# Kernel optimization log

Measured on AMD Instinct MI355X. Metric: run time of the kernel, lower is better.

The kernel has to match this reference:

```python
import jax, jax.numpy as jnp
import numpy as np

EPS = 1e-7  # keras backend.epsilon()
NUM_ROUTING = 3


def squash(v, axis=-1):
    s2 = jnp.sum(jnp.square(v), axis=axis, keepdims=True)
    scale = s2 / (1.0 + s2) / jnp.sqrt(s2 + EPS)
    return scale * v


def setup_inputs() -> dict:
    key = jax.random.key(0)
    k1, k2 = jax.random.split(key)
    B, J, I, P, Q = 64, 32, 2048, 32, 16
    inputs = jax.random.normal(k1, (B, I, Q), dtype=jnp.float32)
    # glorot_uniform for W [J, I, P, Q]
    fan_in, fan_out = Q, P
    limit = np.sqrt(6.0 / (fan_in + fan_out))
    W = jax.random.uniform(k2, (J, I, P, Q), dtype=jnp.float32, minval=-limit, maxval=limit)
    return {"inputs": inputs, "W": W}


def reference(inputs, W):
    # prediction vectors: u_hat[b,j,i,p] = sum_q inputs[b,i,q] * W[j,i,p,q]
    inputs_hat = jnp.einsum('biq,jipq->bjip', inputs, W)  # [B,J,I,P]
    inputs_hat_stop = jax.lax.stop_gradient(inputs_hat)
    B, J, I, _ = inputs_hat.shape
    b = jnp.zeros((B, J, I), dtype=inputs_hat.dtype)
    for _ in range(NUM_ROUTING - 1):
        c = jax.nn.softmax(b, axis=1)  # softmax over output capsules j
        v = squash(jnp.einsum('bji,bjip->bjp', c, inputs_hat_stop))
        b = b + jnp.einsum('bjp,bjip->bji', v, inputs_hat_stop)
    c = jax.nn.softmax(b, axis=1)
    return squash(jnp.einsum('bji,bjip->bjp', c, inputs_hat))  # [B,J,P]
```

## Files before the change

kernel.cpp:

```cpp
#include <hip/hip_runtime.h>


namespace {

using bfrag = __attribute__((ext_vector_type(8))) short;
using ffrag = __attribute__((ext_vector_type(4))) float;

constexpr int I_DIM = 2048;
constexpr int B_DIM = 64;
constexpr int N_DIM = 1024;
constexpr int TI    = 16;

__device__ __forceinline__ unsigned short f2bf(float f) {
    unsigned int u = __float_as_uint(f);
    unsigned int r = (u + 0x7fffu + ((u >> 16) & 1u)) >> 16;
    return (unsigned short)r;
}

template<int CTRL>
__device__ __forceinline__ float dppf(float x) {
    return __int_as_float(
        __builtin_amdgcn_update_dpp(0, __float_as_int(x), CTRL, 0xF, 0xF, true));
}
__device__ __forceinline__ float sum16(float x) {
    x += dppf<0x121>(x);
    x += dppf<0x122>(x);
    x += dppf<0x124>(x);
    x += dppf<0x128>(x);
    return x;
}
__device__ __forceinline__ float max16(float x) {
    x = fmaxf(x, dppf<0x121>(x));
    x = fmaxf(x, dppf<0x122>(x));
    x = fmaxf(x, dppf<0x124>(x));
    x = fmaxf(x, dppf<0x128>(x));
    return x;
}


__global__ __launch_bounds__(256)
void conv_w(const float* __restrict__ W, unsigned short* __restrict__ Wt) {
    const int t = blockIdx.x * 256 + threadIdx.x;
    const int i = t >> 10, n = t & 1023;
    const float* src = W + ((((n >> 5) * I_DIM + i) * 32 + (n & 31)) << 4);
    unsigned int o[8];
    #pragma unroll
    for (int k = 0; k < 8; ++k)
        o[k] = (unsigned int)f2bf(src[2 * k]) | ((unsigned int)f2bf(src[2 * k + 1]) << 16);
    uint4* dst = reinterpret_cast<uint4*>(Wt + (size_t)t * 16);
    dst[0] = make_uint4(o[0], o[1], o[2], o[3]);
    dst[1] = make_uint4(o[4], o[5], o[6], o[7]);
}

__global__ __launch_bounds__(256)
void conv_x(const float* __restrict__ x, unsigned short* __restrict__ xT2) {
    const int t = blockIdx.x * 256 + threadIdx.x;
    const int i = t >> 6, b = t & 63;
    const float* src = x + (((size_t)b * I_DIM + i) << 4);
    unsigned int o[16];
    #pragma unroll
    for (int k = 0; k < 8; ++k) {
        const float f0 = src[2 * k], f1 = src[2 * k + 1];
        const unsigned short h0 = f2bf(f0), h1 = f2bf(f1);
        const float l0 = f0 - __uint_as_float(((unsigned int)h0) << 16);
        const float l1 = f1 - __uint_as_float(((unsigned int)h1) << 16);
        o[k]     = (unsigned int)h0       | ((unsigned int)h1 << 16);
        o[8 + k] = (unsigned int)f2bf(l0) | ((unsigned int)f2bf(l1) << 16);
    }
    uint4* dst = reinterpret_cast<uint4*>(xT2 + (size_t)t * 32);
    #pragma unroll
    for (int k = 0; k < 4; ++k)
        dst[k] = make_uint4(o[4 * k], o[4 * k + 1], o[4 * k + 2], o[4 * k + 3]);
}

#define LOAD_FRAGS(iv)                                                          \
    do {                                                                        \
        const int i_ = (iv);                                                    \
        af = *reinterpret_cast<const bfrag*>(                                   \
            xT2 + (((size_t)i_ << 6) + b0 + li) * 32 + g8);                     \
        _Pragma("unroll")                                                       \
        for (int t = 0; t < 4; ++t)                                             \
            bfr[t] = *reinterpret_cast<const bfrag*>(                           \
                Wt + (((size_t)i_ << 10) + ((j0 + (t >> 1)) << 5)               \
                      + ((t & 1) << 4) + li) * 16 + qb);                        \
    } while (0)

template<bool ROUTED>
__global__ __launch_bounds__(1024, 4)
void caps_pass(const unsigned short* __restrict__ Wt,
               const unsigned short* __restrict__ xT2,
               const float* __restrict__ v_in,
               float* __restrict__ s_out)
{
    __shared__ float d_buf[16 * 33];
    __shared__ float c_buf[16 * 33];

    const int tid = threadIdx.x;
    const int w   = tid >> 6;
    const int l   = tid & 63;
    const int g   = l >> 4;
    const int li  = l & 15;
    const int j0  = w << 1;
    const int qb  = (g & 1) << 3;
    const int g8  = g << 3;

    const int bid = (int)blockIdx.x;
    const int V   = (bid & 7) * 64 + (bid >> 3);
    const int it  = V >> 2;
    const int b0  = (V & 3) << 4;

    float vr[4][4];
    if (ROUTED) {
        #pragma unroll
        for (int r = 0; r < 4; ++r)
            #pragma unroll
            for (int t = 0; t < 4; ++t)
                vr[r][t] = v_in[((b0 + (g << 2) + r) * 32 + j0 + (t >> 1)) * 32
                                + ((t & 1) << 4) + li];
    }

    bfrag af;
    bfrag bfr[4];
    LOAD_FRAGS(it * TI);

    ffrag s[4];
    #pragma unroll
    for (int t = 0; t < 4; ++t) s[t] = ffrag{0.f, 0.f, 0.f, 0.f};

    for (int ii = 0; ii < TI; ++ii) {
        ffrag u[4];
        #pragma unroll
        for (int t = 0; t < 4; ++t) {
            ffrag z{0.f, 0.f, 0.f, 0.f};
            u[t] = __builtin_amdgcn_mfma_f32_16x16x32_bf16(af, bfr[t], z, 0, 0, 0);
        }

        LOAD_FRAGS(it * TI + ((ii + 1 < TI) ? (ii + 1) : ii));
        asm volatile("" ::: "memory");

        if (ROUTED) {
            float dsel[4];
            #pragma unroll
            for (int r = 0; r < 4; ++r) {
                float d0 = u[0][r] * vr[r][0] + u[1][r] * vr[r][1];
                float d1 = u[2][r] * vr[r][2] + u[3][r] * vr[r][3];
                d0 = sum16(d0);
                d1 = sum16(d1);
                dsel[r] = (li & 1) ? d1 : d0;
            }
            #pragma unroll
            for (int r = 0; r < 4; ++r)
                if (li < 2) d_buf[((g << 2) + r) * 33 + j0 + li] = dsel[r];

            asm volatile("s_waitcnt lgkmcnt(0)\n\ts_barrier" ::: "memory");

            if (tid < 512) {
                const int bl = tid >> 5, jx = tid & 31;
                const float bn = d_buf[bl * 33 + jx];
                float m = max16(bn);
                m = fmaxf(m, __shfl_xor(m, 16));
                const float e = __expf(bn - m);
                float ssum = sum16(e);
                ssum += __shfl_xor(ssum, 16);
                c_buf[bl * 33 + jx] = e / ssum;
            }

            asm volatile("s_waitcnt lgkmcnt(0)\n\ts_barrier" ::: "memory");

            #pragma unroll
            for (int r = 0; r < 4; ++r) {
                const float c0 = c_buf[((g << 2) + r) * 33 + j0];
                const float c1 = c_buf[((g << 2) + r) * 33 + j0 + 1];
                s[0][r] += c0 * u[0][r];
                s[1][r] += c0 * u[1][r];
                s[2][r] += c1 * u[2][r];
                s[3][r] += c1 * u[3][r];
            }
        } else {
            #pragma unroll
            for (int t = 0; t < 4; ++t) s[t] += u[t];
        }
    }

    const float sc = ROUTED ? 1.f : (1.f / 32.f);
    #pragma unroll
    for (int t = 0; t < 4; ++t)
        #pragma unroll
        for (int r = 0; r < 4; ++r)
            atomicAdd(&s_out[(b0 + (g << 2) + r) * N_DIM
                             + ((j0 + (t >> 1)) << 5) + ((t & 1) << 4) + li],
                      s[t][r] * sc);
}

__global__ __launch_bounds__(256)
void squash_add(const float* __restrict__ s, const float* __restrict__ base,
                float* __restrict__ dst) {
    const int t = blockIdx.x * 256 + threadIdx.x;
    if (t >= B_DIM * 32) return;
    const float* sp = s + t * 32;
    float n2 = 0.f;
    #pragma unroll
    for (int p = 0; p < 32; ++p) { const float xv = sp[p]; n2 += xv * xv; }
    const float scl = n2 / ((1.f + n2) * sqrtf(n2 + 1e-7f));
    float* op = dst + t * 32;
    #pragma unroll
    for (int p = 0; p < 32; ++p)
        op[p] = (base ? base[t * 32 + p] : 0.f) + scl * sp[p];
}

}

extern "C" void kernel_launch(void* const* d_in, const int* in_sizes, int n_in,
                              void* d_out, int out_size, void* d_ws, size_t ws_size,
                              hipStream_t stream) {
    const float* x = (const float*)d_in[0];
    const float* W = (const float*)d_in[1];
    float* out = (float*)d_out;

    const size_t needW = (size_t)I_DIM * N_DIM * 16 * 2;
    const size_t needX = (size_t)I_DIM * B_DIM * 32 * 2;
    const size_t needS = (size_t)B_DIM * N_DIM * 4;

    char* p = (char*)d_ws;
    unsigned short* Wt  = (unsigned short*)p; p += needW;
    unsigned short* xT2 = (unsigned short*)p; p += needX;
    float* s  = (float*)p; p += needS;
    float* v1 = (float*)p; p += needS;
    float* vs = (float*)p;

    conv_x<<<(I_DIM * B_DIM) / 256, 256, 0, stream>>>(x, xT2);
    conv_w<<<(I_DIM * N_DIM) / 256, 256, 0, stream>>>(W, Wt);

    const dim3 rg(512), rb(1024);

    hipMemsetAsync(s, 0, needS, stream);
    caps_pass<false><<<rg, rb, 0, stream>>>(Wt, xT2, nullptr, s);
    squash_add<<<8, 256, 0, stream>>>(s, nullptr, v1);

    hipMemsetAsync(s, 0, needS, stream);
    caps_pass<true><<<rg, rb, 0, stream>>>(Wt, xT2, v1, s);
    squash_add<<<8, 256, 0, stream>>>(s, v1, vs);

    hipMemsetAsync(s, 0, needS, stream);
    caps_pass<true><<<rg, rb, 0, stream>>>(Wt, xT2, vs, s);
    squash_add<<<8, 256, 0, stream>>>(s, nullptr, out);
}
```

Before: 255.5 us.

## Fuse W bf16 conversion into first pass, batch routing by two i, drop atomics

The separate conv_w kernel is removed. The first (unrouted) capsule pass now reads fp32 W directly, converts it to bf16 in registers, and writes the converted tiles for later passes. Routed passes process two i-rows per barrier pair to halve synchronisation, and a 1024-thread softmax covers 32 rows. Atomic accumulation and the memsets are replaced by per-tile partial sums that a new squash_reduce kernel sums, at the cost of a 32MB partial buffer written and read each pass.

```diff
diff --git a/kernel.cpp b/kernel.cpp
--- a/kernel.cpp
+++ b/kernel.cpp
@@ -10,11 +10,11 @@
 constexpr int B_DIM = 64;
 constexpr int N_DIM = 1024;
 constexpr int TI    = 16;
+constexpr int NIT   = I_DIM / TI;
 
 __device__ __forceinline__ unsigned short f2bf(float f) {
     unsigned int u = __float_as_uint(f);
-    unsigned int r = (u + 0x7fffu + ((u >> 16) & 1u)) >> 16;
-    return (unsigned short)r;
+    return (unsigned short)((u + 0x7fffu + ((u >> 16) & 1u)) >> 16);
 }
 
 template<int CTRL>
@@ -23,33 +23,14 @@
         __builtin_amdgcn_update_dpp(0, __float_as_int(x), CTRL, 0xF, 0xF, true));
 }
 __device__ __forceinline__ float sum16(float x) {
-    x += dppf<0x121>(x);
-    x += dppf<0x122>(x);
-    x += dppf<0x124>(x);
-    x += dppf<0x128>(x);
+    x += dppf<0x121>(x); x += dppf<0x122>(x);
+    x += dppf<0x124>(x); x += dppf<0x128>(x);
     return x;
 }
 __device__ __forceinline__ float max16(float x) {
-    x = fmaxf(x, dppf<0x121>(x));
-    x = fmaxf(x, dppf<0x122>(x));
-    x = fmaxf(x, dppf<0x124>(x));
-    x = fmaxf(x, dppf<0x128>(x));
+    x = fmaxf(x, dppf<0x121>(x)); x = fmaxf(x, dppf<0x122>(x));
+    x = fmaxf(x, dppf<0x124>(x)); x = fmaxf(x, dppf<0x128>(x));
     return x;
-}
-
-
-__global__ __launch_bounds__(256)
-void conv_w(const float* __restrict__ W, unsigned short* __restrict__ Wt) {
-    const int t = blockIdx.x * 256 + threadIdx.x;
-    const int i = t >> 10, n = t & 1023;
-    const float* src = W + ((((n >> 5) * I_DIM + i) * 32 + (n & 31)) << 4);
-    unsigned int o[8];
-    #pragma unroll
-    for (int k = 0; k < 8; ++k)
-        o[k] = (unsigned int)f2bf(src[2 * k]) | ((unsigned int)f2bf(src[2 * k + 1]) << 16);
-    uint4* dst = reinterpret_cast<uint4*>(Wt + (size_t)t * 16);
-    dst[0] = make_uint4(o[0], o[1], o[2], o[3]);
-    dst[1] = make_uint4(o[4], o[5], o[6], o[7]);
 }
 
 __global__ __launch_bounds__(256)
@@ -73,27 +54,16 @@
         dst[k] = make_uint4(o[4 * k], o[4 * k + 1], o[4 * k + 2], o[4 * k + 3]);
 }
 
-#define LOAD_FRAGS(iv)                                                          \
-    do {                                                                        \
-        const int i_ = (iv);                                                    \
-        af = *reinterpret_cast<const bfrag*>(                                   \
-            xT2 + (((size_t)i_ << 6) + b0 + li) * 32 + g8);                     \
-        _Pragma("unroll")                                                       \
-        for (int t = 0; t < 4; ++t)                                             \
-            bfr[t] = *reinterpret_cast<const bfrag*>(                           \
-                Wt + (((size_t)i_ << 10) + ((j0 + (t >> 1)) << 5)               \
-                      + ((t & 1) << 4) + li) * 16 + qb);                        \
-    } while (0)
-
 template<bool ROUTED>
-__global__ __launch_bounds__(1024, 4)
-void caps_pass(const unsigned short* __restrict__ Wt,
+__global__ __launch_bounds__(1024)
+void caps_pass(const float* __restrict__ Wf,
+               unsigned short* __restrict__ Wt,
                const unsigned short* __restrict__ xT2,
                const float* __restrict__ v_in,
-               float* __restrict__ s_out)
+               float* __restrict__ s_part)
 {
-    __shared__ float d_buf[16 * 33];
-    __shared__ float c_buf[16 * 33];
+    __shared__ float d_buf[32 * 33];
+    __shared__ float c_buf[32 * 33];
 
     const int tid = threadIdx.x;
     const int w   = tid >> 6;
@@ -109,76 +79,120 @@
     const int it  = V >> 2;
     const int b0  = (V & 3) << 4;
 
-    float vr[4][4];
-    if (ROUTED) {
+    const unsigned short* pa = xT2 + (b0 + li) * 32 + g8;
+
+    ffrag s[4];
+    #pragma unroll
+    for (int t = 0; t < 4; ++t) s[t] = ffrag{0.f, 0.f, 0.f, 0.f};
+
+    if constexpr (ROUTED) {
+        float vr[4][4];
         #pragma unroll
         for (int r = 0; r < 4; ++r)
             #pragma unroll
             for (int t = 0; t < 4; ++t)
                 vr[r][t] = v_in[((b0 + (g << 2) + r) * 32 + j0 + (t >> 1)) * 32
                                 + ((t & 1) << 4) + li];
-    }
-
-    bfrag af;
-    bfrag bfr[4];
-    LOAD_FRAGS(it * TI);
-
-    ffrag s[4];
-    #pragma unroll
-    for (int t = 0; t < 4; ++t) s[t] = ffrag{0.f, 0.f, 0.f, 0.f};
-
-    for (int ii = 0; ii < TI; ++ii) {
-        ffrag u[4];
-        #pragma unroll
-        for (int t = 0; t < 4; ++t) {
-            ffrag z{0.f, 0.f, 0.f, 0.f};
-            u[t] = __builtin_amdgcn_mfma_f32_16x16x32_bf16(af, bfr[t], z, 0, 0, 0);
+
+        const unsigned short* pb[4];
+        #pragma unroll
+        for (int t = 0; t < 4; ++t)
+            pb[t] = Wt + (size_t)((((j0 + (t >> 1)) << 5) + ((t & 1) << 4) + li) * 16 + qb);
+
+        bfrag afn[2], bfn[2][4];
+        #pragma unroll
+        for (int ic = 0; ic < 2; ++ic) {
+            const size_t i0 = (size_t)(it * TI + ic);
+            afn[ic] = *reinterpret_cast<const bfrag*>(pa + (i0 << 11));
+            #pragma unroll
+            for (int t = 0; t < 4; ++t)
+                bfn[ic][t] = *reinterpret_cast<const bfrag*>(pb[t] + (i0 << 14));
         }
 
-        LOAD_FRAGS(it * TI + ((ii + 1 < TI) ? (ii + 1) : ii));
-        asm volatile("" ::: "memory");
-
-        if (ROUTED) {
-            float dsel[4];
-            #pragma unroll
-            for (int r = 0; r < 4; ++r) {
-                float d0 = u[0][r] * vr[r][0] + u[1][r] * vr[r][1];
-                float d1 = u[2][r] * vr[r][2] + u[3][r] * vr[r][3];
-                d0 = sum16(d0);
-                d1 = sum16(d1);
-                dsel[r] = (li & 1) ? d1 : d0;
+        for (int cc = 0; cc < TI / 2; ++cc) {
+            ffrag u[2][4];
+            #pragma unroll
+            for (int ic = 0; ic < 2; ++ic)
+                #pragma unroll
+                for (int t = 0; t < 4; ++t) {
+                    ffrag z{0.f, 0.f, 0.f, 0.f};
+                    u[ic][t] = __builtin_amdgcn_mfma_f32_16x16x32_bf16(
+                        afn[ic], bfn[ic][t], z, 0, 0, 0);
+                }
+
+            const int inext = it * TI + ((cc < TI / 2 - 1) ? 2 * cc + 2 : 2 * cc);
+            #pragma unroll
+            for (int ic = 0; ic < 2; ++ic) {
+                const size_t i0 = (size_t)(inext + ic);
+                afn[ic] = *reinterpret_cast<const bfrag*>(pa + (i0 << 11));
+                #pragma unroll
+                for (int t = 0; t < 4; ++t)
+                    bfn[ic][t] = *reinterpret_cast<const bfrag*>(pb[t] + (i0 << 14));
             }
-            #pragma unroll
-            for (int r = 0; r < 4; ++r)
-                if (li < 2) d_buf[((g << 2) + r) * 33 + j0 + li] = dsel[r];
+            asm volatile("" ::: "memory");
+
+            #pragma unroll
+            for (int ic = 0; ic < 2; ++ic)
+                #pragma unroll
+                for (int r = 0; r < 4; ++r) {
+                    float d0 = u[ic][0][r] * vr[r][0] + u[ic][1][r] * vr[r][1];
+                    float d1 = u[ic][2][r] * vr[r][2] + u[ic][3][r] * vr[r][3];
+                    d0 = sum16(d0);
+                    d1 = sum16(d1);
+                    const float dsel = (li & 1) ? d1 : d0;
+                    if (li < 2)
+                        d_buf[((ic << 4) + (g << 2) + r) * 33 + j0 + li] = dsel;
+                }
 
             asm volatile("s_waitcnt lgkmcnt(0)\n\ts_barrier" ::: "memory");
 
-            if (tid < 512) {
-                const int bl = tid >> 5, jx = tid & 31;
-                const float bn = d_buf[bl * 33 + jx];
+            {
+                const int row = tid >> 5, jx = tid & 31;
+                const float bn = d_buf[row * 33 + jx];
                 float m = max16(bn);
                 m = fmaxf(m, __shfl_xor(m, 16));
                 const float e = __expf(bn - m);
                 float ssum = sum16(e);
                 ssum += __shfl_xor(ssum, 16);
-                c_buf[bl * 33 + jx] = e / ssum;
+                c_buf[row * 33 + jx] = e / ssum;
             }
 
             asm volatile("s_waitcnt lgkmcnt(0)\n\ts_barrier" ::: "memory");
 
             #pragma unroll
-            for (int r = 0; r < 4; ++r) {
-                const float c0 = c_buf[((g << 2) + r) * 33 + j0];
-                const float c1 = c_buf[((g << 2) + r) * 33 + j0 + 1];
-                s[0][r] += c0 * u[0][r];
-                s[1][r] += c0 * u[1][r];
-                s[2][r] += c1 * u[2][r];
-                s[3][r] += c1 * u[3][r];
+            for (int ic = 0; ic < 2; ++ic)
+                #pragma unroll
+                for (int r = 0; r < 4; ++r) {
+                    const float c0 = c_buf[((ic << 4) + (g << 2) + r) * 33 + j0];
+                    const float c1 = c_buf[((ic << 4) + (g << 2) + r) * 33 + j0 + 1];
+                    s[0][r] += c0 * u[ic][0][r];
+                    s[1][r] += c0 * u[ic][1][r];
+                    s[2][r] += c1 * u[ic][2][r];
+                    s[3][r] += c1 * u[ic][3][r];
+                }
+        }
+    } else {
+        for (int ii = 0; ii < TI; ++ii) {
+            const int i = it * TI + ii;
+            const bfrag a = *reinterpret_cast<const bfrag*>(pa + ((size_t)i << 11));
+            #pragma unroll
+            for (int t = 0; t < 4; ++t) {
+                const int jj = j0 + (t >> 1);
+                const int nl = ((t & 1) << 4) + li;
+                const float* wp = Wf + (((size_t)jj * I_DIM + i) << 9) + nl * 16 + qb;
+                const float4 wa = reinterpret_cast<const float4*>(wp)[0];
+                const float4 wb = reinterpret_cast<const float4*>(wp)[1];
+                bfrag bf;
+                bf[0] = (short)f2bf(wa.x); bf[1] = (short)f2bf(wa.y);
+                bf[2] = (short)f2bf(wa.z); bf[3] = (short)f2bf(wa.w);
+                bf[4] = (short)f2bf(wb.x); bf[5] = (short)f2bf(wb.y);
+                bf[6] = (short)f2bf(wb.z); bf[7] = (short)f2bf(wb.w);
+                if (b0 == 0 && g < 2) {
+                    *reinterpret_cast<bfrag*>(
+                        Wt + ((((size_t)i << 10) + (jj << 5) + nl) << 4) + qb) = bf;
+                }
+                s[t] = __builtin_amdgcn_mfma_f32_16x16x32_bf16(a, bf, s[t], 0, 0, 0);
             }
-        } else {
-            #pragma unroll
-            for (int t = 0; t < 4; ++t) s[t] += u[t];
         }
     }
 
@@ -187,25 +201,32 @@
     for (int t = 0; t < 4; ++t)
         #pragma unroll
         for (int r = 0; r < 4; ++r)
-            atomicAdd(&s_out[(b0 + (g << 2) + r) * N_DIM
-                             + ((j0 + (t >> 1)) << 5) + ((t & 1) << 4) + li],
-                      s[t][r] * sc);
+            s_part[((size_t)it * B_DIM + b0 + (g << 2) + r) * N_DIM
+                   + ((j0 + (t >> 1)) << 5) + ((t & 1) << 4) + li] = s[t][r] * sc;
 }
 
 __global__ __launch_bounds__(256)
-void squash_add(const float* __restrict__ s, const float* __restrict__ base,
-                float* __restrict__ dst) {
-    const int t = blockIdx.x * 256 + threadIdx.x;
-    if (t >= B_DIM * 32) return;
-    const float* sp = s + t * 32;
-    float n2 = 0.f;
-    #pragma unroll
-    for (int p = 0; p < 32; ++p) { const float xv = sp[p]; n2 += xv * xv; }
+void squash_reduce(const float* __restrict__ s_part,
+                   const float* __restrict__ base,
+                   float* __restrict__ dst) {
+    const int tid = threadIdx.x;
+    const int rr  = blockIdx.x * 8 + (tid >> 5);
+    const int p   = tid & 31;
+    const int b   = rr >> 5, j = rr & 31;
+    const float* sp = s_part + (size_t)b * N_DIM + (j << 5) + p;
+    float a0 = 0.f, a1 = 0.f, a2 = 0.f, a3 = 0.f;
+    for (int it2 = 0; it2 < NIT; it2 += 4) {
+        a0 += sp[(size_t)(it2 + 0) << 16];
+        a1 += sp[(size_t)(it2 + 1) << 16];
+        a2 += sp[(size_t)(it2 + 2) << 16];
+        a3 += sp[(size_t)(it2 + 3) << 16];
+    }
+    const float sv = (a0 + a1) + (a2 + a3);
+    float n2 = sv * sv;
+    n2 = sum16(n2);
+    n2 += __shfl_xor(n2, 16);
     const float scl = n2 / ((1.f + n2) * sqrtf(n2 + 1e-7f));
-    float* op = dst + t * 32;
-    #pragma unroll
-    for (int p = 0; p < 32; ++p)
-        op[p] = (base ? base[t * 32 + p] : 0.f) + scl * sp[p];
+    dst[rr * 32 + p] = (base ? base[rr * 32 + p] : 0.f) + scl * sv;
 }
 
 }
@@ -219,29 +240,28 @@
 
     const size_t needW = (size_t)I_DIM * N_DIM * 16 * 2;
     const size_t needX = (size_t)I_DIM * B_DIM * 32 * 2;
-    const size_t needS = (size_t)B_DIM * N_DIM * 4;
-
-    char* p = (char*)d_ws;
-    unsigned short* Wt  = (unsigned short*)p; p += needW;
-    unsigned short* xT2 = (unsigned short*)p; p += needX;
-    float* s  = (float*)p; p += needS;
-    float* v1 = (float*)p; p += needS;
-    float* vs = (float*)p;
+    const size_t needP = (size_t)NIT * B_DIM * N_DIM * 4;
+    const size_t needV = (size_t)B_DIM * N_DIM * 4;
+
+    char* pp = (char*)d_ws;
+    unsigned short* Wt  = (unsigned short*)pp; pp += needW;
+    unsigned short* xT2 = (unsigned short*)pp; pp += needX;
+    float* s_part = (float*)pp; pp += needP;
+    float* v1     = (float*)pp; pp += needV;
+    float* vs     = (float*)pp;
+    (void)needX; (void)ws_size;
 
     conv_x<<<(I_DIM * B_DIM) / 256, 256, 0, stream>>>(x, xT2);
-    conv_w<<<(I_DIM * N_DIM) / 256, 256, 0, stream>>>(W, Wt);
 
     const dim3 rg(512), rb(1024);
-
-    hipMemsetAsync(s, 0, needS, stream);
-    caps_pass<false><<<rg, rb, 0, stream>>>(Wt, xT2, nullptr, s);
-    squash_add<<<8, 256, 0, stream>>>(s, nullptr, v1);
-
-    hipMemsetAsync(s, 0, needS, stream);
-    caps_pass<true><<<rg, rb, 0, stream>>>(Wt, xT2, v1, s);
-    squash_add<<<8, 256, 0, stream>>>(s, v1, vs);
-
-    hipMemsetAsync(s, 0, needS, stream);
-    caps_pass<true><<<rg, rb, 0, stream>>>(Wt, xT2, vs, s);
-    squash_add<<<8, 256, 0, stream>>>(s, nullptr, out);
-}
+    const dim3 qg(256), qb(256);
+
+    caps_pass<false><<<rg, rb, 0, stream>>>(W, Wt, xT2, nullptr, s_part);
+    squash_reduce<<<qg, qb, 0, stream>>>(s_part, nullptr, v1);
+
+    caps_pass<true><<<rg, rb, 0, stream>>>(W, Wt, xT2, v1, s_part);
+    squash_reduce<<<qg, qb, 0, stream>>>(s_part, v1, vs);
+
+    caps_pass<true><<<rg, rb, 0, stream>>>(W, Wt, xT2, vs, s_part);
+    squash_reduce<<<qg, qb, 0, stream>>>(s_part, nullptr, out);
+}
```

Result: slower. 335.0 us (+31.1%).

## Split routed pass into agreement, softmax, and weighted-sum sweeps without block barriers

Applied to the files above, without the earlier changes.

The routed pass used to compute agreement, softmax over output capsules, and the weighted sum inside one kernel, with two block barriers per input-capsule step. It is now split into three kernels. The first computes agreement logits and writes them to a global buffer, a separate kernel applies the softmax, and the second sweep recomputes the prediction vectors and accumulates them with the precomputed coefficients. This removes the per-step barriers and shared-memory traffic. In exchange it makes one extra full MFMA sweep over W per routing iteration and adds round trips through several MB of global memory. The unrouted pass also now accumulates directly in the MFMA accumulator, and addressing uses precomputed base pointers.

```diff
diff --git a/kernel.cpp b/kernel.cpp
--- a/kernel.cpp
+++ b/kernel.cpp
@@ -13,8 +13,7 @@
 
 __device__ __forceinline__ unsigned short f2bf(float f) {
     unsigned int u = __float_as_uint(f);
-    unsigned int r = (u + 0x7fffu + ((u >> 16) & 1u)) >> 16;
-    return (unsigned short)r;
+    return (unsigned short)((u + 0x7fffu + ((u >> 16) & 1u)) >> 16);
 }
 
 template<int CTRL>
@@ -23,17 +22,13 @@
         __builtin_amdgcn_update_dpp(0, __float_as_int(x), CTRL, 0xF, 0xF, true));
 }
 __device__ __forceinline__ float sum16(float x) {
-    x += dppf<0x121>(x);
-    x += dppf<0x122>(x);
-    x += dppf<0x124>(x);
-    x += dppf<0x128>(x);
+    x += dppf<0x121>(x); x += dppf<0x122>(x);
+    x += dppf<0x124>(x); x += dppf<0x128>(x);
     return x;
 }
 __device__ __forceinline__ float max16(float x) {
-    x = fmaxf(x, dppf<0x121>(x));
-    x = fmaxf(x, dppf<0x122>(x));
-    x = fmaxf(x, dppf<0x124>(x));
-    x = fmaxf(x, dppf<0x128>(x));
+    x = fmaxf(x, dppf<0x121>(x)); x = fmaxf(x, dppf<0x122>(x));
+    x = fmaxf(x, dppf<0x124>(x)); x = fmaxf(x, dppf<0x128>(x));
     return x;
 }
 
@@ -75,26 +70,22 @@
 
 #define LOAD_FRAGS(iv)                                                          \
     do {                                                                        \
-        const int i_ = (iv);                                                    \
-        af = *reinterpret_cast<const bfrag*>(                                   \
-            xT2 + (((size_t)i_ << 6) + b0 + li) * 32 + g8);                     \
+        const size_t i_ = (size_t)(iv);                                         \
+        af = *reinterpret_cast<const bfrag*>(pa + (i_ << 11));                  \
         _Pragma("unroll")                                                       \
         for (int t = 0; t < 4; ++t)                                             \
-            bfr[t] = *reinterpret_cast<const bfrag*>(                           \
-                Wt + (((size_t)i_ << 10) + ((j0 + (t >> 1)) << 5)               \
-                      + ((t & 1) << 4) + li) * 16 + qb);                        \
+            bfr[t] = *reinterpret_cast<const bfrag*>(pb[t] + (i_ << 14));       \
     } while (0)
 
-template<bool ROUTED>
-__global__ __launch_bounds__(1024, 4)
-void caps_pass(const unsigned short* __restrict__ Wt,
-               const unsigned short* __restrict__ xT2,
-               const float* __restrict__ v_in,
-               float* __restrict__ s_out)
+template<int MODE>
+__global__ __launch_bounds__(1024)
+void caps_sweep(const unsigned short* __restrict__ Wt,
+                const unsigned short* __restrict__ xT2,
+                const float* __restrict__ v_in,
+                const float* __restrict__ c_in,
+                float* __restrict__ d_out,
+                float* __restrict__ s_out)
 {
-    __shared__ float d_buf[16 * 33];
-    __shared__ float c_buf[16 * 33];
-
     const int tid = threadIdx.x;
     const int w   = tid >> 6;
     const int l   = tid & 63;
@@ -109,8 +100,14 @@
     const int it  = V >> 2;
     const int b0  = (V & 3) << 4;
 
+    const unsigned short* pa = xT2 + (b0 + li) * 32 + g8;
+    const unsigned short* pb[4];
+    #pragma unroll
+    for (int t = 0; t < 4; ++t)
+        pb[t] = Wt + (size_t)((((j0 + (t >> 1)) << 5) + ((t & 1) << 4) + li) * 16 + qb);
+
     float vr[4][4];
-    if (ROUTED) {
+    if (MODE == 1) {
         #pragma unroll
         for (int r = 0; r < 4; ++r)
             #pragma unroll
@@ -128,68 +125,79 @@
     for (int t = 0; t < 4; ++t) s[t] = ffrag{0.f, 0.f, 0.f, 0.f};
 
     for (int ii = 0; ii < TI; ++ii) {
-        ffrag u[4];
+        const int i = it * TI + ii;
+
+        float2 cw[4];
+        if (MODE == 2) {
+            #pragma unroll
+            for (int r = 0; r < 4; ++r)
+                cw[r] = *reinterpret_cast<const float2*>(
+                    c_in + ((size_t)i * B_DIM + b0 + (g << 2) + r) * 32 + j0);
+        }
+
+        if (MODE == 0) {
+            #pragma unroll
+            for (int t = 0; t < 4; ++t)
+                s[t] = __builtin_amdgcn_mfma_f32_16x16x32_bf16(af, bfr[t], s[t], 0, 0, 0);
+            LOAD_FRAGS(it * TI + ((ii + 1 < TI) ? ii + 1 : ii));
+            asm volatile("" ::: "memory");
+        } else {
+            ffrag u[4];
+            #pragma unroll
+            for (int t = 0; t < 4; ++t) {
+                ffrag z{0.f, 0.f, 0.f, 0.f};
+                u[t] = __builtin_amdgcn_mfma_f32_16x16x32_bf16(af, bfr[t], z, 0, 0, 0);
+            }
+            LOAD_FRAGS(it * TI + ((ii + 1 < TI) ? ii + 1 : ii));
+            asm volatile("" ::: "memory");
+
+            if (MODE == 1) {
+                #pragma unroll
+                for (int r = 0; r < 4; ++r) {
+                    float d0 = u[0][r] * vr[r][0] + u[1][r] * vr[r][1];
+                    float d1 = u[2][r] * vr[r][2] + u[3][r] * vr[r][3];
+                    d0 = sum16(d0);
+                    d1 = sum16(d1);
+                    const float dsel = (li & 1) ? d1 : d0;
+                    if (li < 2)
+                        d_out[((size_t)i * B_DIM + b0 + (g << 2) + r) * 32 + j0 + li] = dsel;
+                }
+            } else {
+                #pragma unroll
+                for (int r = 0; r < 4; ++r) {
+                    s[0][r] += cw[r].x * u[0][r];
+                    s[1][r] += cw[r].x * u[1][r];
+                    s[2][r] += cw[r].y * u[2][r];
+                    s[3][r] += cw[r].y * u[3][r];
+                }
+            }
+        }
+    }
+
+    if (MODE != 1) {
+        const float sc = (MODE == 0) ? (1.f / 32.f) : 1.f;
         #pragma unroll
-        for (int t = 0; t < 4; ++t) {
-            ffrag z{0.f, 0.f, 0.f, 0.f};
-            u[t] = __builtin_amdgcn_mfma_f32_16x16x32_bf16(af, bfr[t], z, 0, 0, 0);
-        }
-
-        LOAD_FRAGS(it * TI + ((ii + 1 < TI) ? (ii + 1) : ii));
-        asm volatile("" ::: "memory");
-
-        if (ROUTED) {
-            float dsel[4];
-            #pragma unroll
-            for (int r = 0; r < 4; ++r) {
-                float d0 = u[0][r] * vr[r][0] + u[1][r] * vr[r][1];
-                float d1 = u[2][r] * vr[r][2] + u[3][r] * vr[r][3];
-                d0 = sum16(d0);
-                d1 = sum16(d1);
-                dsel[r] = (li & 1) ? d1 : d0;
-            }
+        for (int t = 0; t < 4; ++t)
             #pragma unroll
             for (int r = 0; r < 4; ++r)
-                if (li < 2) d_buf[((g << 2) + r) * 33 + j0 + li] = dsel[r];
-
-            asm volatile("s_waitcnt lgkmcnt(0)\n\ts_barrier" ::: "memory");
-
-            if (tid < 512) {
-                const int bl = tid >> 5, jx = tid & 31;
-                const float bn = d_buf[bl * 33 + jx];
-                float m = max16(bn);
-                m = fmaxf(m, __shfl_xor(m, 16));
-                const float e = __expf(bn - m);
-                float ssum = sum16(e);
-                ssum += __shfl_xor(ssum, 16);
-                c_buf[bl * 33 + jx] = e / ssum;
-            }
-
-            asm volatile("s_waitcnt lgkmcnt(0)\n\ts_barrier" ::: "memory");
-
-            #pragma unroll
-            for (int r = 0; r < 4; ++r) {
-                const float c0 = c_buf[((g << 2) + r) * 33 + j0];
-                const float c1 = c_buf[((g << 2) + r) * 33 + j0 + 1];
-                s[0][r] += c0 * u[0][r];
-                s[1][r] += c0 * u[1][r];
-                s[2][r] += c1 * u[2][r];
-                s[3][r] += c1 * u[3][r];
-            }
-        } else {
-            #pragma unroll
-            for (int t = 0; t < 4; ++t) s[t] += u[t];
-        }
-    }
-
-    const float sc = ROUTED ? 1.f : (1.f / 32.f);
-    #pragma unroll
-    for (int t = 0; t < 4; ++t)
-        #pragma unroll
-        for (int r = 0; r < 4; ++r)
-            atomicAdd(&s_out[(b0 + (g << 2) + r) * N_DIM
-                             + ((j0 + (t >> 1)) << 5) + ((t & 1) << 4) + li],
-                      s[t][r] * sc);
+                atomicAdd(&s_out[(b0 + (g << 2) + r) * N_DIM
+                                 + ((j0 + (t >> 1)) << 5) + ((t & 1) << 4) + li],
+                          s[t][r] * sc);
+    }
+}
+
+__global__ __launch_bounds__(1024)
+void softmax_c(const float* __restrict__ d, float* __restrict__ c) {
+    const int tid = threadIdx.x;
+    const size_t row = (size_t)blockIdx.x * 32 + (tid >> 5);
+    const int jx = tid & 31;
+    const float bn = d[row * 32 + jx];
+    float m = max16(bn);
+    m = fmaxf(m, __shfl_xor(m, 16));
+    const float e = __expf(bn - m);
+    float ssum = sum16(e);
+    ssum += __shfl_xor(ssum, 16);
+    c[row * 32 + jx] = e / ssum;
 }
 
 __global__ __launch_bounds__(256)
@@ -219,29 +227,38 @@
 
     const size_t needW = (size_t)I_DIM * N_DIM * 16 * 2;
     const size_t needX = (size_t)I_DIM * B_DIM * 32 * 2;
+    const size_t needD = (size_t)I_DIM * B_DIM * 32 * 4;
     const size_t needS = (size_t)B_DIM * N_DIM * 4;
 
-    char* p = (char*)d_ws;
-    unsigned short* Wt  = (unsigned short*)p; p += needW;
-    unsigned short* xT2 = (unsigned short*)p; p += needX;
-    float* s  = (float*)p; p += needS;
-    float* v1 = (float*)p; p += needS;
-    float* vs = (float*)p;
+    char* pp = (char*)d_ws;
+    unsigned short* Wt  = (unsigned short*)pp; pp += needW;
+    unsigned short* xT2 = (unsigned short*)pp; pp += needX;
+    float* dbuf = (float*)pp; pp += needD;
+    float* cbuf = (float*)pp; pp += needD;
+    float* s    = (float*)pp; pp += needS;
+    float* v1   = (float*)pp; pp += needS;
+    float* vs   = (float*)pp;
+    (void)ws_size;
 
     conv_x<<<(I_DIM * B_DIM) / 256, 256, 0, stream>>>(x, xT2);
     conv_w<<<(I_DIM * N_DIM) / 256, 256, 0, stream>>>(W, Wt);
 
     const dim3 rg(512), rb(1024);
+    const dim3 sg(I_DIM * B_DIM / 32), sb(1024);
 
     hipMemsetAsync(s, 0, needS, stream);
-    caps_pass<false><<<rg, rb, 0, stream>>>(Wt, xT2, nullptr, s);
+    caps_sweep<0><<<rg, rb, 0, stream>>>(Wt, xT2, nullptr, nullptr, nullptr, s);
     squash_add<<<8, 256, 0, stream>>>(s, nullptr, v1);
 
+    caps_sweep<1><<<rg, rb, 0, stream>>>(Wt, xT2, v1, nullptr, dbuf, nullptr);
+    softmax_c<<<sg, sb, 0, stream>>>(dbuf, cbuf);
     hipMemsetAsync(s, 0, needS, stream);
-    caps_pass<true><<<rg, rb, 0, stream>>>(Wt, xT2, v1, s);
+    caps_sweep<2><<<rg, rb, 0, stream>>>(Wt, xT2, nullptr, cbuf, nullptr, s);
     squash_add<<<8, 256, 0, stream>>>(s, v1, vs);
 
+    caps_sweep<1><<<rg, rb, 0, stream>>>(Wt, xT2, vs, nullptr, dbuf, nullptr);
+    softmax_c<<<sg, sb, 0, stream>>>(dbuf, cbuf);
     hipMemsetAsync(s, 0, needS, stream);
-    caps_pass<true><<<rg, rb, 0, stream>>>(Wt, xT2, vs, s);
+    caps_sweep<2><<<rg, rb, 0, stream>>>(Wt, xT2, nullptr, cbuf, nullptr, s);
     squash_add<<<8, 256, 0, stream>>>(s, nullptr, out);
 }
```

New measurement: 354.2 us. +38.6%, slower.

## Stage W and x tiles into LDS with async double-buffered global_load_lds

Applied to the files above, without the earlier changes.

Replaces per-wave direct global fragment loads with a double-buffered LDS staging pipeline that uses global_load_lds, and repacks W and x in the conversion kernels so each stage is a contiguous copy. Blocks shrink to 512 threads, with each wave handling 4 output capsules (8 MFMA tiles). The unrouted pass now accumulates directly through the MFMA accumulator, and the softmax is spread across all waves. The aim is to hide global memory latency and reduce redundant fragment loads, at the cost of more LDS, more registers and manual vmcnt bookkeeping.

```diff
diff --git a/kernel.cpp b/kernel.cpp
--- a/kernel.cpp
+++ b/kernel.cpp
@@ -13,8 +13,7 @@
 
 __device__ __forceinline__ unsigned short f2bf(float f) {
     unsigned int u = __float_as_uint(f);
-    unsigned int r = (u + 0x7fffu + ((u >> 16) & 1u)) >> 16;
-    return (unsigned short)r;
+    return (unsigned short)((u + 0x7fffu + ((u >> 16) & 1u)) >> 16);
 }
 
 template<int CTRL>
@@ -23,18 +22,26 @@
         __builtin_amdgcn_update_dpp(0, __float_as_int(x), CTRL, 0xF, 0xF, true));
 }
 __device__ __forceinline__ float sum16(float x) {
-    x += dppf<0x121>(x);
-    x += dppf<0x122>(x);
-    x += dppf<0x124>(x);
-    x += dppf<0x128>(x);
+    x += dppf<0x121>(x); x += dppf<0x122>(x);
+    x += dppf<0x124>(x); x += dppf<0x128>(x);
     return x;
 }
 __device__ __forceinline__ float max16(float x) {
-    x = fmaxf(x, dppf<0x121>(x));
-    x = fmaxf(x, dppf<0x122>(x));
-    x = fmaxf(x, dppf<0x124>(x));
-    x = fmaxf(x, dppf<0x128>(x));
+    x = fmaxf(x, dppf<0x121>(x)); x = fmaxf(x, dppf<0x122>(x));
+    x = fmaxf(x, dppf<0x124>(x)); x = fmaxf(x, dppf<0x128>(x));
     return x;
+}
+
+__device__ __forceinline__ void gl2lds16(const void* gsrc, void* ldst) {
+    __builtin_amdgcn_global_load_lds(
+        (const __attribute__((address_space(1))) void*)gsrc,
+        (__attribute__((address_space(3))) void*)ldst, 16, 0, 0);
+}
+
+__device__ __forceinline__ void barrier_lgkm() {
+    asm volatile("s_waitcnt lgkmcnt(0)" ::: "memory");
+    __builtin_amdgcn_s_barrier();
+    __builtin_amdgcn_sched_barrier(0);
 }
 
 
@@ -47,9 +54,10 @@
     #pragma unroll
     for (int k = 0; k < 8; ++k)
         o[k] = (unsigned int)f2bf(src[2 * k]) | ((unsigned int)f2bf(src[2 * k + 1]) << 16);
-    uint4* dst = reinterpret_cast<uint4*>(Wt + (size_t)t * 16);
-    dst[0] = make_uint4(o[0], o[1], o[2], o[3]);
-    dst[1] = make_uint4(o[4], o[5], o[6], o[7]);
+    uint4* d0 = reinterpret_cast<uint4*>(Wt + (((size_t)i * 2 + 0) * 1024 + n) * 8);
+    uint4* d1 = reinterpret_cast<uint4*>(Wt + (((size_t)i * 2 + 1) * 1024 + n) * 8);
+    *d0 = make_uint4(o[0], o[1], o[2], o[3]);
+    *d1 = make_uint4(o[4], o[5], o[6], o[7]);
 }
 
 __global__ __launch_bounds__(256)
@@ -67,129 +75,147 @@
         o[k]     = (unsigned int)h0       | ((unsigned int)h1 << 16);
         o[8 + k] = (unsigned int)f2bf(l0) | ((unsigned int)f2bf(l1) << 16);
     }
-    uint4* dst = reinterpret_cast<uint4*>(xT2 + (size_t)t * 32);
-    #pragma unroll
-    for (int k = 0; k < 4; ++k)
-        dst[k] = make_uint4(o[4 * k], o[4 * k + 1], o[4 * k + 2], o[4 * k + 3]);
-}
-
-#define LOAD_FRAGS(iv)                                                          \
-    do {                                                                        \
-        const int i_ = (iv);                                                    \
-        af = *reinterpret_cast<const bfrag*>(                                   \
-            xT2 + (((size_t)i_ << 6) + b0 + li) * 32 + g8);                     \
-        _Pragma("unroll")                                                       \
-        for (int t = 0; t < 4; ++t)                                             \
-            bfr[t] = *reinterpret_cast<const bfrag*>(                           \
-                Wt + (((size_t)i_ << 10) + ((j0 + (t >> 1)) << 5)               \
-                      + ((t & 1) << 4) + li) * 16 + qb);                        \
-    } while (0)
-
-template<bool ROUTED>
-__global__ __launch_bounds__(1024, 4)
-void caps_pass(const unsigned short* __restrict__ Wt,
-               const unsigned short* __restrict__ xT2,
-               const float* __restrict__ v_in,
-               float* __restrict__ s_out)
+    #pragma unroll
+    for (int g = 0; g < 4; ++g) {
+        uint4* dst = reinterpret_cast<uint4*>(xT2 + (((size_t)i * 4 + g) * 64 + b) * 8);
+        *dst = make_uint4(o[4 * g], o[4 * g + 1], o[4 * g + 2], o[4 * g + 3]);
+    }
+}
+
+#define WAITC() do { if (w == 7) asm volatile("s_waitcnt vmcnt(5)" ::: "memory"); \
+                     else        asm volatile("s_waitcnt vmcnt(4)" ::: "memory"); } while (0)
+
+template<int ROUTED>
+__global__ __launch_bounds__(512, 2)
+void caps_fused(const unsigned short* __restrict__ Wt,
+                const unsigned short* __restrict__ xT2,
+                const float* __restrict__ v_in,
+                float* __restrict__ s_out)
 {
-    __shared__ float d_buf[16 * 33];
-    __shared__ float c_buf[16 * 33];
+    __shared__ short wbuf[2][16384];
+    __shared__ short xbuf[2][512];
+    __shared__ float d_buf[16 * 36];
+    __shared__ float c_buf[16 * 36];
 
     const int tid = threadIdx.x;
     const int w   = tid >> 6;
     const int l   = tid & 63;
     const int g   = l >> 4;
     const int li  = l & 15;
-    const int j0  = w << 1;
-    const int qb  = (g & 1) << 3;
-    const int g8  = g << 3;
+    const int j0  = w << 2;
 
     const int bid = (int)blockIdx.x;
     const int V   = (bid & 7) * 64 + (bid >> 3);
     const int it  = V >> 2;
     const int b0  = (V & 3) << 4;
-
-    float vr[4][4];
+    const int i0  = it * TI;
+
+    float vr[4][8];
     if (ROUTED) {
         #pragma unroll
         for (int r = 0; r < 4; ++r)
             #pragma unroll
-            for (int t = 0; t < 4; ++t)
+            for (int t = 0; t < 8; ++t)
                 vr[r][t] = v_in[((b0 + (g << 2) + r) * 32 + j0 + (t >> 1)) * 32
                                 + ((t & 1) << 4) + li];
-    }
-
-    bfrag af;
-    bfrag bfr[4];
-    LOAD_FRAGS(it * TI);
-
-    ffrag s[4];
-    #pragma unroll
-    for (int t = 0; t < 4; ++t) s[t] = ffrag{0.f, 0.f, 0.f, 0.f};
+        asm volatile("s_waitcnt vmcnt(0)" ::: "memory");
+    }
+
+    auto stage = [&](int i, int bufn) {
+        const unsigned short* wsrc = Wt + ((size_t)i << 14);
+        #pragma unroll
+        for (int k = 0; k < 4; ++k) {
+            const int c = (w << 2) + k;
+            gl2lds16(wsrc + (c << 9) + (l << 3), &wbuf[bufn][c << 9]);
+        }
+        if (w == 7)
+            gl2lds16(xT2 + (((size_t)i << 2) + (l >> 4)) * 512 + ((b0 + (l & 15)) << 3),
+                     &xbuf[bufn][0]);
+    };
+
+    stage(i0, 0);
+    stage(i0 + 1, 1);
+    WAITC();
+    __builtin_amdgcn_s_barrier();
+    __builtin_amdgcn_sched_barrier(0);
+
+    ffrag s[8];
+    #pragma unroll
+    for (int t = 0; t < 8; ++t) s[t] = ffrag{0.f, 0.f, 0.f, 0.f};
 
     for (int ii = 0; ii < TI; ++ii) {
-        ffrag u[4];
-        #pragma unroll
-        for (int t = 0; t < 4; ++t) {
-            ffrag z{0.f, 0.f, 0.f, 0.f};
-            u[t] = __builtin_amdgcn_mfma_f32_16x16x32_bf16(af, bfr[t], z, 0, 0, 0);
-        }
-
-        LOAD_FRAGS(it * TI + ((ii + 1 < TI) ? (ii + 1) : ii));
-        asm volatile("" ::: "memory");
+        const int cur = ii & 1;
+
+        const bfrag a = *reinterpret_cast<const bfrag*>(&xbuf[cur][((g << 4) + li) << 3]);
+        ffrag u[8];
+        #pragma unroll
+        for (int t = 0; t < 8; ++t) {
+            const int n0 = ((j0 + (t >> 1)) << 5) + ((t & 1) << 4);
+            const bfrag bt = *reinterpret_cast<const bfrag*>(
+                &wbuf[cur][((g & 1) << 13) + ((n0 + li) << 3)]);
+            if (ROUTED) {
+                ffrag z{0.f, 0.f, 0.f, 0.f};
+                u[t] = __builtin_amdgcn_mfma_f32_16x16x32_bf16(a, bt, z, 0, 0, 0);
+            } else {
+                s[t] = __builtin_amdgcn_mfma_f32_16x16x32_bf16(a, bt, s[t], 0, 0, 0);
+            }
+        }
 
         if (ROUTED) {
-            float dsel[4];
             #pragma unroll
             for (int r = 0; r < 4; ++r) {
                 float d0 = u[0][r] * vr[r][0] + u[1][r] * vr[r][1];
                 float d1 = u[2][r] * vr[r][2] + u[3][r] * vr[r][3];
-                d0 = sum16(d0);
-                d1 = sum16(d1);
-                dsel[r] = (li & 1) ? d1 : d0;
+                float d2 = u[4][r] * vr[r][4] + u[5][r] * vr[r][5];
+                float d3 = u[6][r] * vr[r][6] + u[7][r] * vr[r][7];
+                d0 = sum16(d0); d1 = sum16(d1); d2 = sum16(d2); d3 = sum16(d3);
+                float sel = d0;
+                sel = (li == 1) ? d1 : sel;
+                sel = (li == 2) ? d2 : sel;
+                sel = (li == 3) ? d3 : sel;
+                if (li < 4) d_buf[((g << 2) + r) * 36 + j0 + li] = sel;
             }
-            #pragma unroll
-            for (int r = 0; r < 4; ++r)
-                if (li < 2) d_buf[((g << 2) + r) * 33 + j0 + li] = dsel[r];
-
-            asm volatile("s_waitcnt lgkmcnt(0)\n\ts_barrier" ::: "memory");
-
-            if (tid < 512) {
-                const int bl = tid >> 5, jx = tid & 31;
-                const float bn = d_buf[bl * 33 + jx];
-                float m = max16(bn);
-                m = fmaxf(m, __shfl_xor(m, 16));
-                const float e = __expf(bn - m);
-                float ssum = sum16(e);
-                ssum += __shfl_xor(ssum, 16);
-                c_buf[bl * 33 + jx] = e / ssum;
-            }
-
-            asm volatile("s_waitcnt lgkmcnt(0)\n\ts_barrier" ::: "memory");
+        }
+        barrier_lgkm();
+
+        if (ii + 2 < TI) stage(i0 + ii + 2, cur);
+
+        if (ROUTED) {
+            const int row = (w << 1) + (l >> 5), jx = l & 31;
+            const float dv = d_buf[row * 36 + jx];
+            float m = max16(dv);
+            m = fmaxf(m, __shfl_xor(m, 16));
+            const float e = __expf(dv - m);
+            float sm = sum16(e);
+            sm += __shfl_xor(sm, 16);
+            c_buf[row * 36 + jx] = e / sm;
+            barrier_lgkm();
 
             #pragma unroll
             for (int r = 0; r < 4; ++r) {
-                const float c0 = c_buf[((g << 2) + r) * 33 + j0];
-                const float c1 = c_buf[((g << 2) + r) * 33 + j0 + 1];
-                s[0][r] += c0 * u[0][r];
-                s[1][r] += c0 * u[1][r];
-                s[2][r] += c1 * u[2][r];
-                s[3][r] += c1 * u[3][r];
+                const ffrag cr = *reinterpret_cast<const ffrag*>(
+                    &c_buf[((g << 2) + r) * 36 + j0]);
+                #pragma unroll
+                for (int t = 0; t < 8; ++t)
+                    s[t][r] += cr[t >> 1] * u[t][r];
             }
-        } else {
-            #pragma unroll
-            for (int t = 0; t < 4; ++t) s[t] += u[t];
-        }
+        }
+
+        if (ii + 2 < TI) WAITC();
+        else             asm volatile("s_waitcnt vmcnt(0)" ::: "memory");
+        __builtin_amdgcn_s_barrier();
+        __builtin_amdgcn_sched_barrier(0);
     }
 
     const float sc = ROUTED ? 1.f : (1.f / 32.f);
     #pragma unroll
-    for (int t = 0; t < 4; ++t)
+    for (int t = 0; t < 8; ++t) {
+        const int n0 = ((j0 + (t >> 1)) << 5) + ((t & 1) << 4);
         #pragma unroll
         for (int r = 0; r < 4; ++r)
-            atomicAdd(&s_out[(b0 + (g << 2) + r) * N_DIM
-                             + ((j0 + (t >> 1)) << 5) + ((t & 1) << 4) + li],
+            atomicAdd(&s_out[(size_t)(b0 + (g << 2) + r) * N_DIM + n0 + li],
                       s[t][r] * sc);
+    }
 }
 
 __global__ __launch_bounds__(256)
@@ -217,31 +243,32 @@
     const float* W = (const float*)d_in[1];
     float* out = (float*)d_out;
 
-    const size_t needW = (size_t)I_DIM * N_DIM * 16 * 2;
-    const size_t needX = (size_t)I_DIM * B_DIM * 32 * 2;
+    const size_t needW = (size_t)I_DIM * 2 * 1024 * 8 * 2;
+    const size_t needX = (size_t)I_DIM * 4 * 64 * 8 * 2;
     const size_t needS = (size_t)B_DIM * N_DIM * 4;
 
-    char* p = (char*)d_ws;
-    unsigned short* Wt  = (unsigned short*)p; p += needW;
-    unsigned short* xT2 = (unsigned short*)p; p += needX;
-    float* s  = (float*)p; p += needS;
-    float* v1 = (float*)p; p += needS;
-    float* vs = (float*)p;
+    char* pp = (char*)d_ws;
+    unsigned short* Wt  = (unsigned short*)pp; pp += needW;
+    unsigned short* xT2 = (unsigned short*)pp; pp += needX;
+    float* s  = (float*)pp; pp += needS;
+    float* v1 = (float*)pp; pp += needS;
+    float* vs = (float*)pp;
+    (void)ws_size;
 
     conv_x<<<(I_DIM * B_DIM) / 256, 256, 0, stream>>>(x, xT2);
     conv_w<<<(I_DIM * N_DIM) / 256, 256, 0, stream>>>(W, Wt);
 
-    const dim3 rg(512), rb(1024);
+    const dim3 rg(512), rb(512);
 
     hipMemsetAsync(s, 0, needS, stream);
-    caps_pass<false><<<rg, rb, 0, stream>>>(Wt, xT2, nullptr, s);
+    caps_fused<0><<<rg, rb, 0, stream>>>(Wt, xT2, nullptr, s);
     squash_add<<<8, 256, 0, stream>>>(s, nullptr, v1);
 
     hipMemsetAsync(s, 0, needS, stream);
-    caps_pass<true><<<rg, rb, 0, stream>>>(Wt, xT2, v1, s);
+    caps_fused<1><<<rg, rb, 0, stream>>>(Wt, xT2, v1, s);
     squash_add<<<8, 256, 0, stream>>>(s, v1, vs);
 
     hipMemsetAsync(s, 0, needS, stream);
-    caps_pass<true><<<rg, rb, 0, stream>>>(Wt, xT2, vs, s);
+    caps_fused<1><<<rg, rb, 0, stream>>>(Wt, xT2, vs, s);
     squash_add<<<8, 256, 0, stream>>>(s, nullptr, out);
 }
```

Result: slower. 286.5 us (+12.1%).
